# Performance work log

Hardware: AMD Instinct MI355X
Metric: run time of the kernel (lower is better)

The kernel has to match this reference:

```python
import jax, jax.numpy as jnp
import numpy as np

NUM_HEADS = 4
GROUPS = 8
EPS = 1e-5

def setup_inputs() -> dict:
    key = jax.random.key(0)
    ks = jax.random.split(key, 4)
    C = 256
    x = jax.random.normal(ks[0], (4, C, 64, 64), dtype=jnp.float32)
    qkv_w = jax.random.normal(ks[1], (3 * C, C), dtype=jnp.float32) * (C ** -0.5)
    qkv_b = jnp.zeros((3 * C,), dtype=jnp.float32)
    proj_w = jax.random.normal(ks[2], (C, C), dtype=jnp.float32) * (C ** -0.5)
    proj_b = jnp.zeros((C,), dtype=jnp.float32)
    gamma = jnp.ones((C,), dtype=jnp.float32)
    beta = jnp.zeros((C,), dtype=jnp.float32)
    return {"x": x, "qkv_w": qkv_w, "qkv_b": qkv_b, "proj_w": proj_w, "proj_b": proj_b, "gamma": gamma, "beta": beta}

def group_norm(x, gamma, beta):
    B, C, H, W = x.shape
    xg = x.reshape(B, GROUPS, C // GROUPS, H, W)
    mean = xg.mean(axis=(2, 3, 4), keepdims=True)
    var = xg.var(axis=(2, 3, 4), keepdims=True)
    xn = (xg - mean) * jax.lax.rsqrt(var + EPS)
    xn = xn.reshape(B, C, H, W)
    return xn * gamma[None, :, None, None] + beta[None, :, None, None]

def reference(x, qkv_w, qkv_b, proj_w, proj_b, gamma, beta):
    B, C, H, W = x.shape
    L = H * W
    hd = C // NUM_HEADS
    xn = group_norm(x, gamma, beta)  # (B,C,H,W)
    xf = xn.reshape(B, C, L)  # tokens along last axis
    # 1x1 conv == per-pixel linear: (3C, C) @ (B, C, L)
    qkv = jnp.einsum('oc,bcl->bol', qkv_w, xf) + qkv_b[None, :, None]
    q, k, v = jnp.split(qkv, 3, axis=1)  # each (B,C,L)
    q = q.reshape(B, NUM_HEADS, hd, L)
    k = k.reshape(B, NUM_HEADS, hd, L)
    v = v.reshape(B, NUM_HEADS, hd, L)
    scale = hd ** -0.5
    attn = jnp.einsum('bhdq,bhdk->bhqk', q, k) * scale
    attn = jax.nn.softmax(attn, axis=-1)
    out = jnp.einsum('bhqk,bhdk->bhdq', attn, v)  # (B,h,hd,L)
    out = out.reshape(B, C, L)
    out = jnp.einsum('oc,bcl->bol', proj_w, out) + proj_b[None, :, None]
    return out.reshape(B, C, H, W) + xn
```

## Files before the change

### kernel.cpp

```cpp
#include <hip/hip_runtime.h>
#include <math.h>

#define L 4096
#define LOG2E_O8 0.18033688011112042f

typedef float f32x16 __attribute__((ext_vector_type(16)));
typedef __bf16 bf16x8 __attribute__((ext_vector_type(8)));

static __device__ __forceinline__ float fast_exp2(float x) {
    return __builtin_amdgcn_exp2f(x);
}
static __device__ __forceinline__ unsigned short f2bfu(float f) {
    unsigned int u = __builtin_bit_cast(unsigned int, f);
    u += 0x7fffu + ((u >> 16) & 1u);
    return (unsigned short)(u >> 16);
}
static __device__ __forceinline__ unsigned int cvtpk(float a, float b) {
    unsigned int r;
    asm("v_cvt_pk_bf16_f32 %0, %1, %2" : "=v"(r) : "v"(a), "v"(b));
    return r;
}
static __device__ __forceinline__ void pl32swap(unsigned int& a, unsigned int& b) {
    auto r = __builtin_amdgcn_permlane32_swap(a, b, false, false);
    a = r[0];
    b = r[1];
}
static __device__ __forceinline__ bf16x8 ld_frag_g(const unsigned short* p) {
    uint4 v = *(const uint4*)p;
    return __builtin_bit_cast(bf16x8, v);
}
static __device__ __forceinline__ bf16x8 ld_frag_s(const unsigned short* p) {
    uint4 v = *(const uint4*)p;
    return __builtin_bit_cast(bf16x8, v);
}

__global__ __launch_bounds__(256) void gn_stats_part_kernel(const float* __restrict__ x,
                                                            float2* __restrict__ part) {
    const int blk = blockIdx.x;
    const float4* p = (const float4*)(x + (size_t)blk * 8192);
    float sum = 0.f, sq = 0.f;
    for (int i = threadIdx.x; i < 2048; i += 256) {
        float4 v = p[i];
        sum += (v.x + v.y) + (v.z + v.w);
        sq  += (v.x * v.x + v.y * v.y) + (v.z * v.z + v.w * v.w);
    }
#pragma unroll
    for (int off = 1; off < 64; off <<= 1) {
        sum += __shfl_xor(sum, off);
        sq  += __shfl_xor(sq, off);
    }
    __shared__ float red[8];
    const int t = threadIdx.x;
    if ((t & 63) == 0) { red[(t >> 6) * 2] = sum; red[(t >> 6) * 2 + 1] = sq; }
    __syncthreads();
    if (t == 0) {
        float s = red[0] + red[2] + red[4] + red[6];
        float q = red[1] + red[3] + red[5] + red[7];
        part[blk] = make_float2(s, q);
    }
}

__global__ __launch_bounds__(64) void gn_stats_final_kernel(const float2* __restrict__ part,
                                                            float2* __restrict__ stats) {
    const int bg = threadIdx.x;
    if (bg < 32) {
        float s = 0.f, q = 0.f;
#pragma unroll
        for (int i = 0; i < 16; ++i) {
            float2 v = part[bg * 16 + i];
            s += v.x; q += v.y;
        }
        const float inv_n = 1.0f / (32.0f * L);
        float mean = s * inv_n;
        float var = q * inv_n - mean * mean;
        stats[bg] = make_float2(mean, rsqrtf(var + 1e-5f));
    }
}

__global__ __launch_bounds__(256) void wcvt_kernel(const float* __restrict__ qkv_w,
                                                   const float* __restrict__ proj_w,
                                                   unsigned short* __restrict__ Wqb,
                                                   unsigned short* __restrict__ Wpb) {
    const int i4 = (blockIdx.x * 256 + threadIdx.x) * 4;
    const float* src;
    unsigned short* dst;
    if (i4 < 196608) { src = qkv_w + i4; dst = Wqb + i4; }
    else             { src = proj_w + (i4 - 196608); dst = Wpb + (i4 - 196608); }
    float4 v = *(const float4*)src;
    ushort4 o;
    o.x = f2bfu(v.x); o.y = f2bfu(v.y); o.z = f2bfu(v.z); o.w = f2bfu(v.w);
    *(ushort4*)dst = o;
}

__global__ __launch_bounds__(256) void gn_apply_kernel(const float* __restrict__ x,
                                                       const float* __restrict__ gamma,
                                                       const float* __restrict__ beta,
                                                       const float2* __restrict__ stats,
                                                       unsigned short* __restrict__ xnT) {
    __shared__ float tile[64][68];
    const int t = threadIdx.x;
    const int b = blockIdx.z, c0 = blockIdx.y * 64, l0 = blockIdx.x * 64;
    const int lc = (t & 15) * 4, cr = t >> 4;
#pragma unroll
    for (int p = 0; p < 4; ++p) {
        const int c = c0 + cr + p * 16;
        const float2 st = stats[b * 8 + (c >> 5)];
        const float g = gamma[c] * st.y;
        const float be = beta[c] - st.x * g;
        float4 v = *(const float4*)&x[((size_t)b * 256 + c) * L + l0 + lc];
        float4 o;
        o.x = v.x * g + be; o.y = v.y * g + be; o.z = v.z * g + be; o.w = v.w * g + be;
        *(float4*)&tile[cr + p * 16][lc] = o;
    }
    __syncthreads();
    const int lr = t >> 2, cc = (t & 3) * 16;
    unsigned short* dst = &xnT[((size_t)b * L + l0 + lr) * 256 + c0 + cc];
#pragma unroll
    for (int g4 = 0; g4 < 4; ++g4) {
        ushort4 o4;
        o4.x = f2bfu(tile[cc + g4 * 4 + 0][lr]);
        o4.y = f2bfu(tile[cc + g4 * 4 + 1][lr]);
        o4.z = f2bfu(tile[cc + g4 * 4 + 2][lr]);
        o4.w = f2bfu(tile[cc + g4 * 4 + 3][lr]);
        *(ushort4*)&dst[g4 * 4] = o4;
    }
}

__global__ __launch_bounds__(256) void qkv_gemm_kernel(
        const unsigned short* __restrict__ xnT,
        const unsigned short* __restrict__ Wq,
        const float* __restrict__ bias,
        unsigned short* __restrict__ Qb,
        unsigned short* __restrict__ Kb,
        unsigned short* __restrict__ Vb) {
    const int t = threadIdx.x, lane = t & 63, w = t >> 6;
    const int l5 = lane >> 5, l31 = lane & 31;
    const int wn = w & 1, wm = w >> 1;
    const int n0 = blockIdx.x * 128 + wn * 64;
    const int m0 = blockIdx.y * 128 + wm * 64;
    const int b = blockIdx.z;
    const unsigned short* ap = xnT + ((size_t)b * L + n0 + l31) * 256 + l5 * 8;
    const unsigned short* bp = Wq + (size_t)(m0 + l31) * 256 + l5 * 8;
    f32x16 acc[2][2];
#pragma unroll
    for (int i = 0; i < 2; ++i)
#pragma unroll
        for (int j = 0; j < 2; ++j)
#pragma unroll
            for (int r = 0; r < 16; ++r) acc[i][j][r] = 0.f;
#pragma unroll
    for (int k0 = 0; k0 < 256; k0 += 16) {
        bf16x8 a0 = ld_frag_g(ap + k0);
        bf16x8 a1 = ld_frag_g(ap + 32 * 256 + k0);
        bf16x8 b0 = ld_frag_g(bp + k0);
        bf16x8 b1 = ld_frag_g(bp + 32 * 256 + k0);
        acc[0][0] = __builtin_amdgcn_mfma_f32_32x32x16_bf16(a0, b0, acc[0][0], 0, 0, 0);
        acc[0][1] = __builtin_amdgcn_mfma_f32_32x32x16_bf16(a0, b1, acc[0][1], 0, 0, 0);
        acc[1][0] = __builtin_amdgcn_mfma_f32_32x32x16_bf16(a1, b0, acc[1][0], 0, 0, 0);
        acc[1][1] = __builtin_amdgcn_mfma_f32_32x32x16_bf16(a1, b1, acc[1][1], 0, 0, 0);
    }
    const int sec = m0 >> 8;
    const size_t bh = (size_t)(b * 4 + ((m0 >> 6) & 3));
#pragma unroll
    for (int j = 0; j < 2; ++j) {
        const int m = m0 + j * 32 + l31;
        const int d = m & 63;
        const float bi = bias[m];
        if (sec < 2) {
            unsigned short* dst = (sec ? Kb : Qb) + bh * L * 64 + d;
            const float sc = (sec == 0) ? LOG2E_O8 : 1.0f;
#pragma unroll
            for (int i = 0; i < 2; ++i)
#pragma unroll
                for (int r = 0; r < 16; ++r) {
                    const int n = n0 + i * 32 + (r & 3) + 8 * (r >> 2) + 4 * l5;
                    dst[(size_t)n * 64] = f2bfu((acc[i][j][r] + bi) * sc);
                }
        } else {
            unsigned short* dst = Vb + (bh * 64 + d) * L;
#pragma unroll
            for (int i = 0; i < 2; ++i)
#pragma unroll
                for (int g = 0; g < 4; ++g) {
                    const int n = n0 + i * 32 + 8 * g + 4 * l5;
                    ushort4 st;
                    st.x = f2bfu(acc[i][j][4 * g + 0] + bi);
                    st.y = f2bfu(acc[i][j][4 * g + 1] + bi);
                    st.z = f2bfu(acc[i][j][4 * g + 2] + bi);
                    st.w = f2bfu(acc[i][j][4 * g + 3] + bi);
                    *(ushort4*)&dst[n] = st;
                }
        }
    }
}

__global__ __launch_bounds__(1024, 4) void attn_kernel(
        const unsigned short* __restrict__ Qb,
        const unsigned short* __restrict__ Kb,
        const unsigned short* __restrict__ Vb,
        unsigned short* __restrict__ aoT) {
    const int t = threadIdx.x;
    const int lane = t & 63, w = t >> 6;
    const int wq = w & 3, wk = w >> 2;
    const int l5 = lane >> 5, l31 = lane & 31;
    const int n = blockIdx.x;
    const int bh_i = n & 15;
    const int qt = n >> 4;
    const int b = bh_i >> 2, h = bh_i & 3;
    const int q0 = qt * 128 + wq * 32;
    const size_t bh = (size_t)bh_i;

    __shared__ alignas(16) char smem[77824];
    auto Kt = (unsigned short(*)[2][32][72])smem;
    auto Vt = (unsigned short(*)[2][64][40])(smem + 36864);
    auto comb = (float(*)[4][64][36])smem;

    const unsigned short* qp = Qb + (bh * L + q0 + l31) * 64 + l5 * 8;
    bf16x8 qf[4];
#pragma unroll
    for (int dc = 0; dc < 4; ++dc) qf[dc] = ld_frag_g(qp + dc * 16);

    const int ts = t & 255;
    const int kr = ts >> 3, kq = ts & 7;
    const int vd = ts >> 2, vp = ts & 3;
    const int kbase = wk * 1024;
    const unsigned short* kgsrc = Kb + bh * L * 64 + (size_t)kbase * 64 + kr * 64 + kq * 8;
    const unsigned short* vgsrc = Vb + (bh * 64 + vd) * L + kbase + vp * 8;

    f32x16 o0, o1;
#pragma unroll
    for (int r2 = 0; r2 < 16; ++r2) { o0[r2] = 0.f; o1[r2] = 0.f; }
    float4 ls = make_float4(0.f, 0.f, 0.f, 0.f);

    {
        uint4 kv = *(const uint4*)kgsrc;
        uint4 vv = *(const uint4*)vgsrc;
        *(uint4*)&Kt[wk][0][kr][kq * 8] = kv;
        *(uint4*)&Vt[wk][0][vd][vp * 8] = vv;
    }
    __syncthreads();

    for (int kc = 0; kc < 32; ++kc) {
        const int buf = kc & 1;
        uint4 knx, vnx;
        if (kc < 31) {
            knx = *(const uint4*)(kgsrc + (size_t)(kc + 1) * 2048);
            vnx = *(const uint4*)(vgsrc + (kc + 1) * 32);
        }
        bf16x8 kf[4], vf[2][2];
#pragma unroll
        for (int dc = 0; dc < 4; ++dc)
            kf[dc] = ld_frag_s(&Kt[wk][buf][l31][dc * 16 + l5 * 8]);
#pragma unroll
        for (int dh = 0; dh < 2; ++dh)
#pragma unroll
            for (int h16 = 0; h16 < 2; ++h16)
                vf[dh][h16] = ld_frag_s(&Vt[wk][buf][dh * 32 + l31][h16 * 16 + l5 * 8]);
        f32x16 s;
#pragma unroll
        for (int r2 = 0; r2 < 16; ++r2) s[r2] = 0.f;
#pragma unroll
        for (int dc = 0; dc < 4; ++dc)
            s = __builtin_amdgcn_mfma_f32_32x32x16_bf16(kf[dc], qf[dc], s, 0, 0, 0);
#pragma unroll
        for (int r2 = 0; r2 < 16; ++r2) s[r2] = fast_exp2(s[r2]);
#pragma unroll
        for (int g = 0; g < 4; ++g) {
            ls.x += s[4 * g + 0];
            ls.y += s[4 * g + 1];
            ls.z += s[4 * g + 2];
            ls.w += s[4 * g + 3];
        }
        unsigned int w0 = cvtpk(s[0],  s[1]);
        unsigned int w1 = cvtpk(s[2],  s[3]);
        unsigned int w2 = cvtpk(s[4],  s[5]);
        unsigned int w3 = cvtpk(s[6],  s[7]);
        unsigned int w4 = cvtpk(s[8],  s[9]);
        unsigned int w5 = cvtpk(s[10], s[11]);
        unsigned int w6 = cvtpk(s[12], s[13]);
        unsigned int w7 = cvtpk(s[14], s[15]);
        pl32swap(w0, w2);
        pl32swap(w1, w3);
        pl32swap(w4, w6);
        pl32swap(w5, w7);
        int4 p0v, p1v;
        p0v.x = (int)w0; p0v.y = (int)w1; p0v.z = (int)w2; p0v.w = (int)w3;
        p1v.x = (int)w4; p1v.y = (int)w5; p1v.z = (int)w6; p1v.w = (int)w7;
        bf16x8 pb0 = __builtin_bit_cast(bf16x8, p0v);
        bf16x8 pb1 = __builtin_bit_cast(bf16x8, p1v);
        o0 = __builtin_amdgcn_mfma_f32_32x32x16_bf16(vf[0][0], pb0, o0, 0, 0, 0);
        o0 = __builtin_amdgcn_mfma_f32_32x32x16_bf16(vf[0][1], pb1, o0, 0, 0, 0);
        o1 = __builtin_amdgcn_mfma_f32_32x32x16_bf16(vf[1][0], pb0, o1, 0, 0, 0);
        o1 = __builtin_amdgcn_mfma_f32_32x32x16_bf16(vf[1][1], pb1, o1, 0, 0, 0);
        if (kc < 31) {
            *(uint4*)&Kt[wk][buf ^ 1][kr][kq * 8] = knx;
            *(uint4*)&Vt[wk][buf ^ 1][vd][vp * 8] = vnx;
        }
        __syncthreads();
    }
    float lrun = (ls.x + ls.y) + (ls.z + ls.w);
    lrun += __shfl_xor(lrun, 32);

    if (wk & 1) {
        float* cb = comb[wk >> 1][wq][lane];
#pragma unroll
        for (int g = 0; g < 4; ++g) {
            *(float4*)&cb[4 * g] =
                make_float4(o0[4 * g + 0], o0[4 * g + 1], o0[4 * g + 2], o0[4 * g + 3]);
            *(float4*)&cb[16 + 4 * g] =
                make_float4(o1[4 * g + 0], o1[4 * g + 1], o1[4 * g + 2], o1[4 * g + 3]);
        }
        cb[32] = lrun;
    }
    __syncthreads();
    if (!(wk & 1)) {
        const float* cb = comb[wk >> 1][wq][lane];
#pragma unroll
        for (int r2 = 0; r2 < 16; ++r2) { o0[r2] += cb[r2]; o1[r2] += cb[16 + r2]; }
        lrun += cb[32];
        if (wk == 2) {
            float* cw = comb[1][wq][lane];
#pragma unroll
            for (int g = 0; g < 4; ++g) {
                *(float4*)&cw[4 * g] =
                    make_float4(o0[4 * g + 0], o0[4 * g + 1], o0[4 * g + 2], o0[4 * g + 3]);
                *(float4*)&cw[16 + 4 * g] =
                    make_float4(o1[4 * g + 0], o1[4 * g + 1], o1[4 * g + 2], o1[4 * g + 3]);
            }
            cw[32] = lrun;
        }
    }
    __syncthreads();
    if (wk == 0) {
        const float* cb = comb[1][wq][lane];
#pragma unroll
        for (int r2 = 0; r2 < 16; ++r2) { o0[r2] += cb[r2]; o1[r2] += cb[16 + r2]; }
        lrun += cb[32];
        const float inv = 1.f / lrun;
        unsigned short* op = aoT + ((size_t)b * L + q0 + l31) * 256 + h * 64 + 4 * l5;
#pragma unroll
        for (int g = 0; g < 4; ++g) {
            uint2 st;
            st.x = cvtpk(o0[4 * g + 0] * inv, o0[4 * g + 1] * inv);
            st.y = cvtpk(o0[4 * g + 2] * inv, o0[4 * g + 3] * inv);
            *(uint2*)&op[8 * g] = st;
            uint2 st2;
            st2.x = cvtpk(o1[4 * g + 0] * inv, o1[4 * g + 1] * inv);
            st2.y = cvtpk(o1[4 * g + 2] * inv, o1[4 * g + 3] * inv);
            *(uint2*)&op[32 + 8 * g] = st2;
        }
    }
}

__global__ __launch_bounds__(256) void proj_gemm_kernel(
        const unsigned short* __restrict__ aoT,
        const unsigned short* __restrict__ Wp,
        const float* __restrict__ bias,
        const float* __restrict__ x,
        const float* __restrict__ gamma,
        const float* __restrict__ beta,
        const float2* __restrict__ stats,
        float* __restrict__ out) {
    const int t = threadIdx.x, lane = t & 63, w = t >> 6;
    const int l5 = lane >> 5, l31 = lane & 31;
    const int wn = w & 1, wm = w >> 1;
    const int n0 = blockIdx.x * 64 + wn * 32;
    const int m0 = blockIdx.y * 128 + wm * 64;
    const int b = blockIdx.z;
    const unsigned short* ap = aoT + ((size_t)b * L + n0 + l31) * 256 + l5 * 8;
    const unsigned short* bp = Wp + (size_t)(m0 + l31) * 256 + l5 * 8;
    f32x16 acc[2];
#pragma unroll
    for (int j = 0; j < 2; ++j)
#pragma unroll
        for (int r = 0; r < 16; ++r) acc[j][r] = 0.f;
#pragma unroll
    for (int k0 = 0; k0 < 256; k0 += 16) {
        bf16x8 a  = ld_frag_g(ap + k0);
        bf16x8 b0 = ld_frag_g(bp + k0);
        bf16x8 b1 = ld_frag_g(bp + 32 * 256 + k0);
        acc[0] = __builtin_amdgcn_mfma_f32_32x32x16_bf16(a, b0, acc[0], 0, 0, 0);
        acc[1] = __builtin_amdgcn_mfma_f32_32x32x16_bf16(a, b1, acc[1], 0, 0, 0);
    }
#pragma unroll
    for (int j = 0; j < 2; ++j) {
        const int co = m0 + j * 32 + l31;
        const float2 st = stats[b * 8 + (co >> 5)];
        const float g = gamma[co] * st.y;
        const float be = beta[co] - st.x * g + bias[co];
        const float* xr = &x[((size_t)b * 256 + co) * L];
        float* orow = &out[((size_t)b * 256 + co) * L];
#pragma unroll
        for (int q = 0; q < 4; ++q) {
            const int n = n0 + 8 * q + 4 * l5;
            float4 xv = *(const float4*)&xr[n];
            float4 ov;
            ov.x = acc[j][4 * q + 0] + (xv.x * g + be);
            ov.y = acc[j][4 * q + 1] + (xv.y * g + be);
            ov.z = acc[j][4 * q + 2] + (xv.z * g + be);
            ov.w = acc[j][4 * q + 3] + (xv.w * g + be);
            *(float4*)&orow[n] = ov;
        }
    }
}

extern "C" void kernel_launch(void* const* d_in, const int* in_sizes, int n_in,
                              void* d_out, int out_size, void* d_ws, size_t ws_size,
                              hipStream_t stream) {
    const float* x      = (const float*)d_in[0];
    const float* qkv_w  = (const float*)d_in[1];
    const float* qkv_b  = (const float*)d_in[2];
    const float* proj_w = (const float*)d_in[3];
    const float* proj_b = (const float*)d_in[4];
    const float* gamma  = (const float*)d_in[5];
    const float* beta   = (const float*)d_in[6];
    float* out = (float*)d_out;

    char* ws = (char*)d_ws;
    float2* stats       = (float2*)ws;
    unsigned short* Wqb = (unsigned short*)(ws + 512);
    unsigned short* Wpb = (unsigned short*)(ws + 512 + 393216);
    unsigned short* xnT = (unsigned short*)(ws + 524800);
    unsigned short* Qb  = (unsigned short*)(ws + 524800 + 8388608);
    unsigned short* Kb  = Qb + (size_t)16 * L * 64;
    unsigned short* Vb  = Kb + (size_t)16 * L * 64;
    unsigned short* aoT = Vb + (size_t)16 * L * 64;
    float2* spart       = (float2*)(ws + 524800);

    gn_stats_part_kernel<<<dim3(512), dim3(256), 0, stream>>>(x, spart);
    gn_stats_final_kernel<<<dim3(1), dim3(64), 0, stream>>>(spart, stats);
    wcvt_kernel<<<dim3(256), dim3(256), 0, stream>>>(qkv_w, proj_w, Wqb, Wpb);
    gn_apply_kernel<<<dim3(64, 4, 4), dim3(256), 0, stream>>>(x, gamma, beta, stats, xnT);
    qkv_gemm_kernel<<<dim3(32, 6, 4), dim3(256), 0, stream>>>(xnT, Wqb, qkv_b, Qb, Kb, Vb);
    attn_kernel<<<dim3(512), dim3(1024), 0, stream>>>(Qb, Kb, Vb, aoT);
    proj_gemm_kernel<<<dim3(64, 2, 4), dim3(256), 0, stream>>>(aoT, Wpb, proj_b, x, gamma, beta, stats, out);
}
```

Measured before the change: 224.2 us.

## Restructure attention to 4-wave blocks with 32 queries and shared K/V tiles

```diff
diff --git a/kernel.cpp b/kernel.cpp
--- a/kernel.cpp
+++ b/kernel.cpp
@@ -194,38 +194,35 @@
     }
 }
 
-__global__ __launch_bounds__(1024, 4) void attn_kernel(
+__global__ __launch_bounds__(256) void attn_kernel(
         const unsigned short* __restrict__ Qb,
         const unsigned short* __restrict__ Kb,
         const unsigned short* __restrict__ Vb,
         unsigned short* __restrict__ aoT) {
     const int t = threadIdx.x;
     const int lane = t & 63, w = t >> 6;
-    const int wq = w & 3, wk = w >> 2;
     const int l5 = lane >> 5, l31 = lane & 31;
     const int n = blockIdx.x;
     const int bh_i = n & 15;
     const int qt = n >> 4;
     const int b = bh_i >> 2, h = bh_i & 3;
-    const int q0 = qt * 128 + wq * 32;
+    const int q0 = qt * 32;
     const size_t bh = (size_t)bh_i;
 
-    __shared__ alignas(16) char smem[77824];
-    auto Kt = (unsigned short(*)[2][32][72])smem;
-    auto Vt = (unsigned short(*)[2][64][40])(smem + 36864);
-    auto comb = (float(*)[4][64][36])smem;
+    __shared__ alignas(16) char smem[68608];
+    auto Kt = (unsigned short(*)[128][68])smem;
+    auto Vt = (unsigned short(*)[64][132])(smem + 34816);
+    auto comb = (float(*)[64][36])smem;
 
     const unsigned short* qp = Qb + (bh * L + q0 + l31) * 64 + l5 * 8;
     bf16x8 qf[4];
 #pragma unroll
     for (int dc = 0; dc < 4; ++dc) qf[dc] = ld_frag_g(qp + dc * 16);
 
-    const int ts = t & 255;
-    const int kr = ts >> 3, kq = ts & 7;
-    const int vd = ts >> 2, vp = ts & 3;
-    const int kbase = wk * 1024;
-    const unsigned short* kgsrc = Kb + bh * L * 64 + (size_t)kbase * 64 + kr * 64 + kq * 8;
-    const unsigned short* vgsrc = Vb + (bh * 64 + vd) * L + kbase + vp * 8;
+    const int ksr = t >> 1, ksp = t & 1;
+    const int vdr = t >> 2, vpp = t & 3;
+    const unsigned short* kgsrc = Kb + bh * L * 64 + ksr * 64 + ksp * 32;
+    const unsigned short* vgsrc = Vb + (bh * 64 + vdr) * L + vpp * 32;
 
     f32x16 o0, o1;
 #pragma unroll
@@ -233,29 +230,39 @@
     float4 ls = make_float4(0.f, 0.f, 0.f, 0.f);
 
     {
-        uint4 kv = *(const uint4*)kgsrc;
-        uint4 vv = *(const uint4*)vgsrc;
-        *(uint4*)&Kt[wk][0][kr][kq * 8] = kv;
-        *(uint4*)&Vt[wk][0][vd][vp * 8] = vv;
+#pragma unroll
+        for (int i = 0; i < 4; ++i) {
+            uint4 kv = *(const uint4*)(kgsrc + i * 8);
+            *(uint4*)&Kt[0][ksr][ksp * 32 + i * 8] = kv;
+        }
+#pragma unroll
+        for (int i = 0; i < 4; ++i) {
+            uint4 vv = *(const uint4*)(vgsrc + i * 8);
+            *(uint4*)&Vt[0][vdr][vpp * 32 + i * 8] = vv;
+        }
     }
     __syncthreads();
 
-    for (int kc = 0; kc < 32; ++kc) {
-        const int buf = kc & 1;
-        uint4 knx, vnx;
-        if (kc < 31) {
-            knx = *(const uint4*)(kgsrc + (size_t)(kc + 1) * 2048);
-            vnx = *(const uint4*)(vgsrc + (kc + 1) * 32);
+    for (int ic = 0; ic < 32; ++ic) {
+        const int buf = ic & 1;
+        uint4 kn[4], vn[4];
+        if (ic < 31) {
+            const unsigned short* kg = kgsrc + (size_t)(ic + 1) * 8192;
+            const unsigned short* vg = vgsrc + (ic + 1) * 128;
+#pragma unroll
+            for (int i = 0; i < 4; ++i) kn[i] = *(const uint4*)(kg + i * 8);
+#pragma unroll
+            for (int i = 0; i < 4; ++i) vn[i] = *(const uint4*)(vg + i * 8);
         }
         bf16x8 kf[4], vf[2][2];
 #pragma unroll
         for (int dc = 0; dc < 4; ++dc)
-            kf[dc] = ld_frag_s(&Kt[wk][buf][l31][dc * 16 + l5 * 8]);
+            kf[dc] = ld_frag_s(&Kt[buf][w * 32 + l31][dc * 16 + l5 * 8]);
 #pragma unroll
         for (int dh = 0; dh < 2; ++dh)
 #pragma unroll
             for (int h16 = 0; h16 < 2; ++h16)
-                vf[dh][h16] = ld_frag_s(&Vt[wk][buf][dh * 32 + l31][h16 * 16 + l5 * 8]);
+                vf[dh][h16] = ld_frag_s(&Vt[buf][dh * 32 + l31][w * 32 + h16 * 16 + l5 * 8]);
         f32x16 s;
 #pragma unroll
         for (int r2 = 0; r2 < 16; ++r2) s[r2] = 0.f;
@@ -292,17 +299,21 @@
         o0 = __builtin_amdgcn_mfma_f32_32x32x16_bf16(vf[0][1], pb1, o0, 0, 0, 0);
         o1 = __builtin_amdgcn_mfma_f32_32x32x16_bf16(vf[1][0], pb0, o1, 0, 0, 0);
         o1 = __builtin_amdgcn_mfma_f32_32x32x16_bf16(vf[1][1], pb1, o1, 0, 0, 0);
-        if (kc < 31) {
-            *(uint4*)&Kt[wk][buf ^ 1][kr][kq * 8] = knx;
-            *(uint4*)&Vt[wk][buf ^ 1][vd][vp * 8] = vnx;
+        if (ic < 31) {
+#pragma unroll
+            for (int i = 0; i < 4; ++i)
+                *(uint4*)&Kt[buf ^ 1][ksr][ksp * 32 + i * 8] = kn[i];
+#pragma unroll
+            for (int i = 0; i < 4; ++i)
+                *(uint4*)&Vt[buf ^ 1][vdr][vpp * 32 + i * 8] = vn[i];
         }
         __syncthreads();
     }
     float lrun = (ls.x + ls.y) + (ls.z + ls.w);
     lrun += __shfl_xor(lrun, 32);
 
-    if (wk & 1) {
-        float* cb = comb[wk >> 1][wq][lane];
+    if (w) {
+        float* cb = comb[w - 1][lane];
 #pragma unroll
         for (int g = 0; g < 4; ++g) {
             *(float4*)&cb[4 * g] =
@@ -313,29 +324,14 @@
         cb[32] = lrun;
     }
     __syncthreads();
-    if (!(wk & 1)) {
-        const float* cb = comb[wk >> 1][wq][lane];
-#pragma unroll
-        for (int r2 = 0; r2 < 16; ++r2) { o0[r2] += cb[r2]; o1[r2] += cb[16 + r2]; }
-        lrun += cb[32];
-        if (wk == 2) {
-            float* cw = comb[1][wq][lane];
-#pragma unroll
-            for (int g = 0; g < 4; ++g) {
-                *(float4*)&cw[4 * g] =
-                    make_float4(o0[4 * g + 0], o0[4 * g + 1], o0[4 * g + 2], o0[4 * g + 3]);
-                *(float4*)&cw[16 + 4 * g] =
-                    make_float4(o1[4 * g + 0], o1[4 * g + 1], o1[4 * g + 2], o1[4 * g + 3]);
-            }
-            cw[32] = lrun;
-        }
-    }
-    __syncthreads();
-    if (wk == 0) {
-        const float* cb = comb[1][wq][lane];
-#pragma unroll
-        for (int r2 = 0; r2 < 16; ++r2) { o0[r2] += cb[r2]; o1[r2] += cb[16 + r2]; }
-        lrun += cb[32];
+    if (w == 0) {
+#pragma unroll
+        for (int p = 0; p < 3; ++p) {
+            const float* cb = comb[p][lane];
+#pragma unroll
+            for (int r2 = 0; r2 < 16; ++r2) { o0[r2] += cb[r2]; o1[r2] += cb[16 + r2]; }
+            lrun += cb[32];
+        }
         const float inv = 1.f / lrun;
         unsigned short* op = aoT + ((size_t)b * L + q0 + l31) * 256 + h * 64 + 4 * l5;
 #pragma unroll
@@ -432,6 +428,6 @@
     wcvt_kernel<<<dim3(256), dim3(256), 0, stream>>>(qkv_w, proj_w, Wqb, Wpb);
     gn_apply_kernel<<<dim3(64, 4, 4), dim3(256), 0, stream>>>(x, gamma, beta, stats, xnT);
     qkv_gemm_kernel<<<dim3(32, 6, 4), dim3(256), 0, stream>>>(xnT, Wqb, qkv_b, Qb, Kb, Vb);
-    attn_kernel<<<dim3(512), dim3(1024), 0, stream>>>(Qb, Kb, Vb, aoT);
+    attn_kernel<<<dim3(2048), dim3(256), 0, stream>>>(Qb, Kb, Vb, aoT);
     proj_gemm_kernel<<<dim3(64, 2, 4), dim3(256), 0, stream>>>(aoT, Wpb, proj_b, x, gamma, beta, stats, out);
 }
```

New measurement: 600.4 us. 168% more time.
